# Kernel optimization log

Hardware: AMD Instinct MI355X
Metric: run time of the kernel (lower is better)

The kernel has to match this reference:

```python
import jax, jax.numpy as jnp
import numpy as np

KAPPA = -1.0          # negative curvature (Poincare ball, c = 1)
EPS = 1e-10
N, D_IN, D_OUT = 8192, 512, 512


def _artan_k(x):
    sc = np.sqrt(-KAPPA)
    return jnp.arctanh(jnp.clip(sc * x, -1.0 + 1e-7, 1.0 - 1e-7)) / sc


def _tan_k(x):
    sc = np.sqrt(-KAPPA)
    return jnp.tanh(sc * x) / sc


def _clamp_abs(x, eps=EPS):
    return jnp.where(x >= 0, 1.0, -1.0) * jnp.maximum(jnp.abs(x), eps)


def _norm(x):
    # stable last-dim L2 norm, clamped away from zero
    return jnp.sqrt(jnp.maximum(jnp.sum(x * x, axis=-1, keepdims=True), EPS * EPS))


def mobius_matvec(W, x):
    # geoopt-style Mobius matrix-vector product: scale x@W so that the
    # gyro-norm matches tan_k((|mx|/|x|) * artan_k(|x|))
    x_norm = _norm(x)                       # [N,1]
    mx = x @ W                              # [N,D_out]
    mx_norm = _norm(mx)
    res = _tan_k(mx_norm / x_norm * _artan_k(x_norm)) * (mx / mx_norm)
    return jnp.where(mx_norm <= EPS, 0.0, res)


def mobius_scalar_mul(r, x):
    x_norm = _norm(x)
    return _tan_k(r * _artan_k(x_norm)) * (x / x_norm)


def weighted_midpoint_lincomb(A, X):
    # weighted Frechet-mean-like midpoint with lincomb=True (geoopt semantics):
    # gamma_i = lambda_x = 2 / (1 + kappa * |x_i|^2)
    gamma = jnp.maximum(2.0 / (1.0 + KAPPA * jnp.sum(X * X, axis=-1, keepdims=True)), 1e-15)  # [N,1]
    denom = _clamp_abs(A @ (gamma - 1.0))   # [N,1]  (sum_j A_ij (gamma_j - 1))
    nom = A @ (gamma * X)                   # [N,D]  (sum_j A_ij gamma_j x_j)  -- GEMM, no NxNxD temp
    two_mean = nom / denom
    sq = jnp.sum(two_mean * two_mean, axis=-1, keepdims=True)
    a_mean = two_mean / (1.0 + jnp.sqrt(jnp.maximum(1.0 + KAPPA * sq, EPS)))
    alpha = jnp.sum(A, axis=-1, keepdims=True)   # lincomb: Mobius-scale by total weight
    return mobius_scalar_mul(alpha, a_mean)


def logmap0(x):
    xn = _norm(x)
    return _artan_k(xn) * x / xn


def expmap0(u):
    un = _norm(u)
    return _tan_k(un) * u / un


def setup_inputs() -> dict:
    key = jax.random.key(0)
    k1, k2, k3 = jax.random.split(key, 3)
    # node embeddings well inside the Poincare ball (|x| ~ 0.02)
    X = jax.random.normal(k1, (N, D_IN), dtype=jnp.float32) * 0.001
    # dense nonnegative normalized adjacency (rows sum ~ 0.5)
    A_hat = jax.random.uniform(k2, (N, N), dtype=jnp.float32) / N
    W = jax.random.normal(k3, (D_IN, D_OUT), dtype=jnp.float32) * 0.01
    return {"X": X, "A_hat": A_hat, "W": W}


def reference(X, A_hat, W):
    XW = mobius_matvec(W, X)                     # Mobius linear layer
    AXW = weighted_midpoint_lincomb(A_hat, XW)   # adjacency-weighted midpoint aggregation
    return expmap0(jax.nn.relu(logmap0(AXW)))    # sigma = exp0(relu(log0(.)))
```

## Files before the change

### kernel.cpp

```cpp
#include <hip/hip_runtime.h>


#define NR 8192
#define DD 512

typedef unsigned int u32;
typedef unsigned short u16;
typedef __attribute__((ext_vector_type(8))) short bf16x8;
typedef __attribute__((ext_vector_type(4))) float f32x4;

__device__ __forceinline__ u16 f2bf(float f) {
  u32 u = __float_as_uint(f);
  u32 r = u + 0x7FFFu + ((u >> 16) & 1u);
  return (u16)(r >> 16);
}

__device__ __forceinline__ u32 cvtpk(float lo, float hi) {
  u32 r;
  asm("v_cvt_pk_bf16_f32 %0, %1, %2" : "=v"(r) : "v"(lo), "v"(hi));
  return r;
}

__device__ __forceinline__ void gload16(const void* g, void* l) {
  __builtin_amdgcn_global_load_lds(
      (const __attribute__((address_space(1))) u32*)g,
      (__attribute__((address_space(3))) u32*)l, 16, 0, 0);
}

__device__ __forceinline__ float wred(float v) {
  #pragma unroll
  for (int off = 32; off; off >>= 1) v += __shfl_xor(v, off, 64);
  return v;
}

__global__ __launch_bounds__(256) void conv_wt(const float* __restrict__ W,
                                               u16* __restrict__ Wt) {
  const int idx = blockIdx.x * 256 + threadIdx.x;
  const int n  = idx >> 6;
  const int k0 = (idx & 63) * 8;
  u32 r[4];
  #pragma unroll
  for (int j = 0; j < 4; ++j) {
    float lo = W[(size_t)(k0 + 2*j    ) * DD + n];
    float hi = W[(size_t)(k0 + 2*j + 1) * DD + n];
    r[j] = (u32)f2bf(lo) | ((u32)f2bf(hi) << 16);
  }
  const int dst = n * DD + ((idx & 63) >> 2) * 32 + (((idx & 3) ^ (n & 3)) * 8);
  *(uint4*)(Wt + dst) = *(const uint4*)r;
}

template <int DOSUM>
__global__ __launch_bounds__(512, 2) void gemm_big(
    const float* __restrict__ Af, const u16* __restrict__ Bt,
    const u16* __restrict__ g1bf,
    float* __restrict__ C0, float* __restrict__ Cext,
    float* __restrict__ denp, float* __restrict__ alp,
    int M, int K, int kchunk, int nkc) {
  __shared__ __align__(16) float ldsA[2][4096];
  __shared__ __align__(16) u16   ldsB[2][16384];
  __shared__ __align__(16) u16   ldsG[2048];

  const int bid = blockIdx.x;
  int mt, kc;
  if (nkc == 1) { mt = bid; kc = 0; }
  else { kc = (bid & 7) >> 1; mt = ((bid >> 3) << 1) | (bid & 1); }

  const int t = threadIdx.x;
  const int lane = t & 63, w = t >> 6;
  const int wm = w >> 2, wn = w & 3;
  const int m0 = mt * 128;
  const int kbeg = kc * kchunk;
  const int lr = lane & 15, lk = lane >> 4, lx = lr & 7;

  const int Rb   = t >> 3;
  const int scol = ((t & 7) ^ (Rb & 7)) << 2;
  const float* gA0 = Af + (size_t)(m0 + Rb) * K + kbeg + scol;

  const u16* gB = Bt + (size_t)(t >> 2) * K + kbeg + (t & 3) * 8;

  auto stage = [&](int buf, int kt) {
    const int ko = kt * 32;
    #pragma unroll
    for (int j = 0; j < 2; ++j)
      gload16(gA0 + ko + (size_t)j * 64 * K, &ldsA[buf][t * 4 + j * 2048]);
    #pragma unroll
    for (int j = 0; j < 4; ++j)
      gload16(gB + ko + (size_t)j * 128 * K, &ldsB[buf][t * 8 + j * 4096]);
  };

  f32x4 acc[4][8];
  #pragma unroll
  for (int i = 0; i < 4; ++i)
    #pragma unroll
    for (int j = 0; j < 8; ++j) acc[i][j] = (f32x4){0.f, 0.f, 0.f, 0.f};
  f32x4 accS[4];
  #pragma unroll
  for (int i = 0; i < 4; ++i) accS[i] = (f32x4){0.f, 0.f, 0.f, 0.f};

  const int nT = kchunk / 32;

  if (DOSUM && w < 4) gload16(g1bf + kbeg + t * 8, &ldsG[t * 8]);
  stage(0, 0);
  stage(1, 1);
  asm volatile("s_waitcnt vmcnt(6)" ::: "memory");
  __builtin_amdgcn_s_barrier();
  __builtin_amdgcn_sched_barrier(0);

  int cur = 0;
  for (int tt = 0; tt < nT; ++tt) {
    bf16x8 af[4], bv[8];
    #pragma unroll
    for (int i = 0; i < 4; ++i) {
      const int rbase = (wm * 64 + i * 16 + lr) * 32;
      f32x4 lo = *(const f32x4*)&ldsA[cur][rbase + (((2*lk    ) ^ lx) << 2)];
      f32x4 hi = *(const f32x4*)&ldsA[cur][rbase + (((2*lk + 1) ^ lx) << 2)];
      union { u32 u[4]; bf16x8 v; } pk;
      pk.u[0] = cvtpk(lo.x, lo.y); pk.u[1] = cvtpk(lo.z, lo.w);
      pk.u[2] = cvtpk(hi.x, hi.y); pk.u[3] = cvtpk(hi.z, hi.w);
      af[i] = pk.v;
    }
    #pragma unroll
    for (int i = 0; i < 8; ++i) {
      const int rb = (wn * 128 + i * 16 + lr) * 32 + ((lk ^ (lr & 3)) << 3);
      bv[i] = *(const bf16x8*)&ldsB[cur][rb];
    }
    bf16x8 gv;
    if (DOSUM && wn == 0) {
      if (lr == 0) {
        gv = *(const bf16x8*)&ldsG[tt * 32 + lk * 8];
      } else {
        const short s = (lr == 1) ? (short)0x3F80 : (short)0;
        gv = (bf16x8){s, s, s, s, s, s, s, s};
      }
    }
    asm volatile("s_waitcnt lgkmcnt(0)" ::: "memory");
    __builtin_amdgcn_s_barrier();
    __builtin_amdgcn_sched_barrier(0);
    if (tt + 2 < nT) stage(cur, tt + 2);
    __builtin_amdgcn_sched_barrier(0);
    #pragma unroll
    for (int mi = 0; mi < 4; ++mi)
      #pragma unroll
      for (int ni = 0; ni < 8; ++ni)
        acc[mi][ni] = __builtin_amdgcn_mfma_f32_16x16x32_bf16(
            af[mi], bv[ni], acc[mi][ni], 0, 0, 0);
    if (DOSUM && wn == 0) {
      #pragma unroll
      for (int i = 0; i < 4; ++i)
        accS[i] = __builtin_amdgcn_mfma_f32_16x16x32_bf16(
            af[i], gv, accS[i], 0, 0, 0);
    }
    if (tt + 1 < nT) {
      __builtin_amdgcn_sched_barrier(0);
      if (tt + 2 < nT) {
        asm volatile("s_waitcnt vmcnt(6)" ::: "memory");
      } else {
        asm volatile("s_waitcnt vmcnt(0)" ::: "memory");
      }
      __builtin_amdgcn_s_barrier();
      __builtin_amdgcn_sched_barrier(0);
    }
    cur ^= 1;
  }

  if (DOSUM && wn == 0 && lr < 2) {
    float* dst = ((lr == 0) ? denp : alp) + (size_t)kc * M + m0 + wm * 64;
    #pragma unroll
    for (int i = 0; i < 4; ++i)
      #pragma unroll
      for (int v = 0; v < 4; ++v)
        dst[i * 16 + lk * 4 + v] = accS[i][v];
  }

  float* C = (kc == 0) ? C0 : (Cext + (size_t)(kc - 1) * M * DD);
  float* Cw = C + (size_t)(m0 + wm * 64 + lk * 4) * DD + wn * 128 + lr;
  #pragma unroll
  for (int mi = 0; mi < 4; ++mi)
    #pragma unroll
    for (int ni = 0; ni < 8; ++ni)
      #pragma unroll
      for (int v = 0; v < 4; ++v)
        Cw[(size_t)(mi * 16 + v) * DD + ni * 16] = acc[mi][ni][v];
}

__global__ __launch_bounds__(256) void rowstats(const float* __restrict__ X,
                                                const float* __restrict__ mx,
                                                float* __restrict__ fg,
                                                u16* __restrict__ g1bf) {
  const int row  = (blockIdx.x << 2) + (threadIdx.x >> 6);
  const int lane = threadIdx.x & 63;
  const float* xr = X  + (size_t)row * DD + lane * 8;
  const float* mr = mx + (size_t)row * DD + lane * 8;
  float4 a0 = *(const float4*)xr, a1 = *(const float4*)(xr + 4);
  float4 b0 = *(const float4*)mr, b1 = *(const float4*)(mr + 4);
  float sx = a0.x*a0.x + a0.y*a0.y + a0.z*a0.z + a0.w*a0.w
           + a1.x*a1.x + a1.y*a1.y + a1.z*a1.z + a1.w*a1.w;
  float sm = b0.x*b0.x + b0.y*b0.y + b0.z*b0.z + b0.w*b0.w
           + b1.x*b1.x + b1.y*b1.y + b1.z*b1.z + b1.w*b1.w;
  sx = wred(sx); sm = wred(sm);
  if (lane == 0) {
    float xn  = sqrtf(fmaxf(sx, 1e-20f));
    float mxn = sqrtf(fmaxf(sm, 1e-20f));
    float at  = atanhf(fminf(xn, 0.9999999f));
    float t_  = tanhf(mxn / xn * at);
    bool  z   = (mxn <= 1e-10f);
    float factor = z ? 0.f : t_ / mxn;
    float xwsq   = z ? 0.f : t_ * t_ * (sm / (mxn * mxn));
    float g = 2.f / (1.f - xwsq);
    g = fmaxf(g, 1e-15f);
    fg[row] = factor * g;
    g1bf[row] = f2bf(g - 1.f);
  }
}

__global__ __launch_bounds__(256) void build_bt(const float* __restrict__ mx,
                                                const float* __restrict__ fg,
                                                u16* __restrict__ Bt) {
  __shared__ float tile[64][65];
  const int j0 = blockIdx.x * 64, d0 = blockIdx.y * 64;
  const int t = threadIdx.x;
  const int r0 = t >> 4, c4 = (t & 15) * 4;
  #pragma unroll
  for (int p = 0; p < 4; ++p) {
    const int r = r0 + p * 16;
    const float s = fg[j0 + r];
    float4 v = *(const float4*)&mx[(size_t)(j0 + r) * DD + d0 + c4];
    tile[r][c4 + 0] = s * v.x; tile[r][c4 + 1] = s * v.y;
    tile[r][c4 + 2] = s * v.z; tile[r][c4 + 3] = s * v.w;
  }
  __syncthreads();
  const int dr = t >> 2, jc = (t & 3) * 16;
  u32 r[8];
  #pragma unroll
  for (int u = 0; u < 8; ++u) {
    float lo = tile[jc + 2 * u][dr];
    float hi = tile[jc + 2 * u + 1][dr];
    r[u] = (u32)f2bf(lo) | ((u32)f2bf(hi) << 16);
  }
  const int s0 = (jc >> 3) & 3;
  const int px = dr & 3;
  u32* rowp = (u32*)(Bt + (size_t)(d0 + dr) * NR + j0 + (jc & 32));
  *(uint4*)(rowp + ((s0 ^ px) * 4))       = *(const uint4*)&r[0];
  *(uint4*)(rowp + (((s0 + 1) ^ px) * 4)) = *(const uint4*)&r[4];
}

__global__ __launch_bounds__(256) void epilogue(const float* __restrict__ P0,
                                                const float* __restrict__ P1,
                                                const float* __restrict__ P2,
                                                const float* __restrict__ P3,
                                                const float* __restrict__ denp,
                                                const float* __restrict__ alp,
                                                float* __restrict__ out) {
  const int row  = (blockIdx.x << 2) + (threadIdx.x >> 6);
  const int lane = threadIdx.x & 63;
  const size_t ro = (size_t)row * DD + lane * 8;
  float4 n0 = *(const float4*)(P0 + ro), n1 = *(const float4*)(P0 + ro + 4);
  float4 a, b;
  a = *(const float4*)(P1 + ro); b = *(const float4*)(P1 + ro + 4);
  n0.x += a.x; n0.y += a.y; n0.z += a.z; n0.w += a.w;
  n1.x += b.x; n1.y += b.y; n1.z += b.z; n1.w += b.w;
  a = *(const float4*)(P2 + ro); b = *(const float4*)(P2 + ro + 4);
  n0.x += a.x; n0.y += a.y; n0.z += a.z; n0.w += a.w;
  n1.x += b.x; n1.y += b.y; n1.z += b.z; n1.w += b.w;
  a = *(const float4*)(P3 + ro); b = *(const float4*)(P3 + ro + 4);
  n0.x += a.x; n0.y += a.y; n0.z += a.z; n0.w += a.w;
  n1.x += b.x; n1.y += b.y; n1.z += b.z; n1.w += b.w;

  float de = 0.f, alpha = 0.f;
  #pragma unroll
  for (int kc = 0; kc < 4; ++kc) {
    de    += denp[kc * NR + row];
    alpha += alp [kc * NR + row];
  }
  de = (de >= 0.f ? 1.f : -1.f) * fmaxf(fabsf(de), 1e-10f);

  float v[8] = {n0.x / de, n0.y / de, n0.z / de, n0.w / de,
                n1.x / de, n1.y / de, n1.z / de, n1.w / de};
  float sq = 0.f;
  #pragma unroll
  for (int j = 0; j < 8; ++j) sq += v[j] * v[j];
  sq = wred(sq);
  float s1 = 1.f + sqrtf(fmaxf(1.f - sq, 1e-10f));
  float an = sqrtf(fmaxf(sq / (s1 * s1), 1e-20f));
  float t2 = tanhf(alpha * atanhf(fminf(an, 0.9999999f)));
  float f2 = t2 / (an * s1);
  float xsq = f2 * f2 * sq;
  float xn = sqrtf(fmaxf(xsq, 1e-20f));
  float lf = atanhf(fminf(xn, 0.9999999f)) / xn;
  float u[8]; float us = 0.f;
  #pragma unroll
  for (int j = 0; j < 8; ++j) {
    u[j] = fmaxf(lf * f2 * v[j], 0.f);
    us += u[j] * u[j];
  }
  us = wred(us);
  float un = sqrtf(fmaxf(us, 1e-20f));
  float ef = tanhf(un) / un;
  float o[8];
  #pragma unroll
  for (int j = 0; j < 8; ++j) o[j] = ef * u[j];
  float* orow = out + (size_t)row * DD + lane * 8;
  *(float4*)orow       = (float4){o[0], o[1], o[2], o[3]};
  *(float4*)(orow + 4) = (float4){o[4], o[5], o[6], o[7]};
}

extern "C" void kernel_launch(void* const* d_in, const int* in_sizes, int n_in,
                              void* d_out, int out_size, void* d_ws, size_t ws_size,
                              hipStream_t stream) {
  const float* X = (const float*)d_in[0];
  const float* A = (const float*)d_in[1];
  const float* W = (const float*)d_in[2];
  float* out = (float*)d_out;
  char* ws = (char*)d_ws;

  float* mx   = (float*)(ws);
  float* Pext = (float*)(ws + 16777216);
  u16*   Bt   = (u16*)(ws + 67108864);
  u16*   Wt   = (u16*)(ws + 75497472);
  float* fg   = (float*)(ws + 76021760);
  u16*   g1bf = (u16*)(ws + 76054528);
  float* denp = (float*)(ws + 76087296);
  float* alp  = (float*)(ws + 76218368);

  const size_t MNf = (size_t)NR * DD;

  conv_wt<<<128, 256, 0, stream>>>(W, Wt);
  gemm_big<0><<<64, 512, 0, stream>>>(X, Wt, g1bf, mx, mx, denp, alp,
                                      NR, DD, DD, 1);
  rowstats<<<2048, 256, 0, stream>>>(X, mx, fg, g1bf);
  build_bt<<<dim3(128, 8), 256, 0, stream>>>(mx, fg, Bt);
  gemm_big<1><<<256, 512, 0, stream>>>(A, Bt, g1bf, mx, Pext, denp, alp,
                                       NR, NR, NR / 4, 4);
  epilogue<<<2048, 256, 0, stream>>>(mx, Pext, Pext + MNf, Pext + 2 * MNf,
                                     denp, alp, out);
}
```

Measured before the change: 201.1 us.

## Split GEMM tiles across N halves, halve split-K, interleave MFMA with staging

The big GEMM now runs 256-thread blocks on 128x256 output tiles, splitting N into two halves and K into two chunks instead of four. This halves the partial-sum buffers the epilogue must read and sum. The main loop is split into two MFMA halves with raised wave priority, and the next tile's loads are issued between them so memory traffic overlaps compute. In exchange, each A tile is now loaded by two blocks (once per N half), which adds A-matrix traffic and changes occupancy.

```diff
diff --git a/kernel.cpp b/kernel.cpp
--- a/kernel.cpp
+++ b/kernel.cpp
@@ -50,42 +50,42 @@
 }
 
 template <int DOSUM>
-__global__ __launch_bounds__(512, 2) void gemm_big(
+__global__ __launch_bounds__(256, 2) void gemm_ph(
     const float* __restrict__ Af, const u16* __restrict__ Bt,
     const u16* __restrict__ g1bf,
     float* __restrict__ C0, float* __restrict__ Cext,
     float* __restrict__ denp, float* __restrict__ alp,
     int M, int K, int kchunk, int nkc) {
   __shared__ __align__(16) float ldsA[2][4096];
-  __shared__ __align__(16) u16   ldsB[2][16384];
-  __shared__ __align__(16) u16   ldsG[2048];
+  __shared__ __align__(16) u16   ldsB[2][8192];
+  __shared__ __align__(16) u16   ldsG[4096];
 
   const int bid = blockIdx.x;
-  int mt, kc;
-  if (nkc == 1) { mt = bid; kc = 0; }
-  else { kc = (bid & 7) >> 1; mt = ((bid >> 3) << 1) | (bid & 1); }
+  const int nt = bid & 1;
+  const int h  = bid >> 1;
+  const int kc = (nkc == 2) ? (h & 1) : 0;
+  const int mt = (nkc == 2) ? (h >> 1) : h;
 
   const int t = threadIdx.x;
   const int lane = t & 63, w = t >> 6;
-  const int wm = w >> 2, wn = w & 3;
-  const int m0 = mt * 128;
+  const int wm = w >> 1, wn = w & 1;
+  const int m0 = mt * 128, n0 = nt * 256;
   const int kbeg = kc * kchunk;
   const int lr = lane & 15, lk = lane >> 4, lx = lr & 7;
-
-  const int Rb   = t >> 3;
-  const int scol = ((t & 7) ^ (Rb & 7)) << 2;
-  const float* gA0 = Af + (size_t)(m0 + Rb) * K + kbeg + scol;
-
-  const u16* gB = Bt + (size_t)(t >> 2) * K + kbeg + (t & 3) * 8;
+  const bool doRS = DOSUM && (nt == 0);
+
+  const int scol = ((t & 7) ^ ((t >> 3) & 7)) << 2;
+  const float* gA0 = Af + (size_t)(m0 + (t >> 3)) * K + kbeg + scol;
+  const u16* gB = Bt + (size_t)(n0 + (t >> 2)) * K + kbeg + (t & 3) * 8;
 
   auto stage = [&](int buf, int kt) {
     const int ko = kt * 32;
     #pragma unroll
-    for (int j = 0; j < 2; ++j)
-      gload16(gA0 + ko + (size_t)j * 64 * K, &ldsA[buf][t * 4 + j * 2048]);
-    #pragma unroll
     for (int j = 0; j < 4; ++j)
-      gload16(gB + ko + (size_t)j * 128 * K, &ldsB[buf][t * 8 + j * 4096]);
+      gload16(gA0 + ko + (size_t)j * 32 * K, &ldsA[buf][t * 4 + j * 1024]);
+    #pragma unroll
+    for (int j = 0; j < 4; ++j)
+      gload16(gB + ko + (size_t)j * 64 * K, &ldsB[buf][t * 8 + j * 2048]);
   };
 
   f32x4 acc[4][8];
@@ -99,10 +99,14 @@
 
   const int nT = kchunk / 32;
 
-  if (DOSUM && w < 4) gload16(g1bf + kbeg + t * 8, &ldsG[t * 8]);
+  if (doRS) {
+    #pragma unroll
+    for (int j = 0; j < 2; ++j)
+      gload16(g1bf + kbeg + t * 8 + j * 2048, &ldsG[t * 8 + j * 2048]);
+  }
   stage(0, 0);
   stage(1, 1);
-  asm volatile("s_waitcnt vmcnt(6)" ::: "memory");
+  asm volatile("s_waitcnt vmcnt(8)" ::: "memory");
   __builtin_amdgcn_s_barrier();
   __builtin_amdgcn_sched_barrier(0);
 
@@ -124,8 +128,21 @@
       const int rb = (wn * 128 + i * 16 + lr) * 32 + ((lk ^ (lr & 3)) << 3);
       bv[i] = *(const bf16x8*)&ldsB[cur][rb];
     }
+    __builtin_amdgcn_s_setprio(1);
+    #pragma unroll
+    for (int mi = 0; mi < 4; ++mi)
+      #pragma unroll
+      for (int ni = 0; ni < 4; ++ni)
+        acc[mi][ni] = __builtin_amdgcn_mfma_f32_16x16x32_bf16(
+            af[mi], bv[ni], acc[mi][ni], 0, 0, 0);
+    __builtin_amdgcn_s_setprio(0);
+    asm volatile("s_waitcnt lgkmcnt(0)" ::: "memory");
+    __builtin_amdgcn_sched_barrier(0);
+    __builtin_amdgcn_s_barrier();
+    __builtin_amdgcn_sched_barrier(0);
+    if (tt + 2 < nT) stage(cur, tt + 2);
     bf16x8 gv;
-    if (DOSUM && wn == 0) {
+    if (doRS && wn == 0) {
       if (lr == 0) {
         gv = *(const bf16x8*)&ldsG[tt * 32 + lk * 8];
       } else {
@@ -133,27 +150,25 @@
         gv = (bf16x8){s, s, s, s, s, s, s, s};
       }
     }
-    asm volatile("s_waitcnt lgkmcnt(0)" ::: "memory");
-    __builtin_amdgcn_s_barrier();
     __builtin_amdgcn_sched_barrier(0);
-    if (tt + 2 < nT) stage(cur, tt + 2);
-    __builtin_amdgcn_sched_barrier(0);
+    __builtin_amdgcn_s_setprio(1);
     #pragma unroll
     for (int mi = 0; mi < 4; ++mi)
       #pragma unroll
-      for (int ni = 0; ni < 8; ++ni)
+      for (int ni = 4; ni < 8; ++ni)
         acc[mi][ni] = __builtin_amdgcn_mfma_f32_16x16x32_bf16(
             af[mi], bv[ni], acc[mi][ni], 0, 0, 0);
-    if (DOSUM && wn == 0) {
+    if (doRS && wn == 0) {
       #pragma unroll
       for (int i = 0; i < 4; ++i)
         accS[i] = __builtin_amdgcn_mfma_f32_16x16x32_bf16(
             af[i], gv, accS[i], 0, 0, 0);
     }
+    __builtin_amdgcn_s_setprio(0);
+    __builtin_amdgcn_sched_barrier(0);
     if (tt + 1 < nT) {
-      __builtin_amdgcn_sched_barrier(0);
-      if (tt + 2 < nT) {
-        asm volatile("s_waitcnt vmcnt(6)" ::: "memory");
+      if (tt + 3 < nT) {
+        asm volatile("s_waitcnt vmcnt(8)" ::: "memory");
       } else {
         asm volatile("s_waitcnt vmcnt(0)" ::: "memory");
       }
@@ -163,7 +178,7 @@
     cur ^= 1;
   }
 
-  if (DOSUM && wn == 0 && lr < 2) {
+  if (doRS && wn == 0 && lr < 2) {
     float* dst = ((lr == 0) ? denp : alp) + (size_t)kc * M + m0 + wm * 64;
     #pragma unroll
     for (int i = 0; i < 4; ++i)
@@ -172,8 +187,8 @@
         dst[i * 16 + lk * 4 + v] = accS[i][v];
   }
 
-  float* C = (kc == 0) ? C0 : (Cext + (size_t)(kc - 1) * M * DD);
-  float* Cw = C + (size_t)(m0 + wm * 64 + lk * 4) * DD + wn * 128 + lr;
+  float* C = (kc == 0) ? C0 : Cext;
+  float* Cw = C + (size_t)(m0 + wm * 64 + lk * 4) * DD + n0 + wn * 128 + lr;
   #pragma unroll
   for (int mi = 0; mi < 4; ++mi)
     #pragma unroll
@@ -246,8 +261,6 @@
 
 __global__ __launch_bounds__(256) void epilogue(const float* __restrict__ P0,
                                                 const float* __restrict__ P1,
-                                                const float* __restrict__ P2,
-                                                const float* __restrict__ P3,
                                                 const float* __restrict__ denp,
                                                 const float* __restrict__ alp,
                                                 float* __restrict__ out) {
@@ -255,23 +268,12 @@
   const int lane = threadIdx.x & 63;
   const size_t ro = (size_t)row * DD + lane * 8;
   float4 n0 = *(const float4*)(P0 + ro), n1 = *(const float4*)(P0 + ro + 4);
-  float4 a, b;
-  a = *(const float4*)(P1 + ro); b = *(const float4*)(P1 + ro + 4);
+  float4 a = *(const float4*)(P1 + ro), b = *(const float4*)(P1 + ro + 4);
   n0.x += a.x; n0.y += a.y; n0.z += a.z; n0.w += a.w;
   n1.x += b.x; n1.y += b.y; n1.z += b.z; n1.w += b.w;
-  a = *(const float4*)(P2 + ro); b = *(const float4*)(P2 + ro + 4);
-  n0.x += a.x; n0.y += a.y; n0.z += a.z; n0.w += a.w;
-  n1.x += b.x; n1.y += b.y; n1.z += b.z; n1.w += b.w;
-  a = *(const float4*)(P3 + ro); b = *(const float4*)(P3 + ro + 4);
-  n0.x += a.x; n0.y += a.y; n0.z += a.z; n0.w += a.w;
-  n1.x += b.x; n1.y += b.y; n1.z += b.z; n1.w += b.w;
-
-  float de = 0.f, alpha = 0.f;
-  #pragma unroll
-  for (int kc = 0; kc < 4; ++kc) {
-    de    += denp[kc * NR + row];
-    alpha += alp [kc * NR + row];
-  }
+
+  float de    = denp[row] + denp[NR + row];
+  float alpha = alp[row]  + alp[NR + row];
   de = (de >= 0.f ? 1.f : -1.f) * fmaxf(fabsf(de), 1e-10f);
 
   float v[8] = {n0.x / de, n0.y / de, n0.z / de, n0.w / de,
@@ -314,23 +316,20 @@
   char* ws = (char*)d_ws;
 
   float* mx   = (float*)(ws);
-  float* Pext = (float*)(ws + 16777216);
-  u16*   Bt   = (u16*)(ws + 67108864);
-  u16*   Wt   = (u16*)(ws + 75497472);
-  float* fg   = (float*)(ws + 76021760);
-  u16*   g1bf = (u16*)(ws + 76054528);
-  float* denp = (float*)(ws + 76087296);
-  float* alp  = (float*)(ws + 76218368);
-
-  const size_t MNf = (size_t)NR * DD;
+  float* P1   = (float*)(ws + 16777216);
+  u16*   Bt   = (u16*)(ws + 33554432);
+  u16*   Wt   = (u16*)(ws + 41943040);
+  float* fg   = (float*)(ws + 42467328);
+  u16*   g1bf = (u16*)(ws + 42500096);
+  float* denp = (float*)(ws + 42516480);
+  float* alp  = (float*)(ws + 42582016);
 
   conv_wt<<<128, 256, 0, stream>>>(W, Wt);
-  gemm_big<0><<<64, 512, 0, stream>>>(X, Wt, g1bf, mx, mx, denp, alp,
+  gemm_ph<0><<<128, 256, 0, stream>>>(X, Wt, g1bf, mx, mx, denp, alp,
                                       NR, DD, DD, 1);
   rowstats<<<2048, 256, 0, stream>>>(X, mx, fg, g1bf);
   build_bt<<<dim3(128, 8), 256, 0, stream>>>(mx, fg, Bt);
-  gemm_big<1><<<256, 512, 0, stream>>>(A, Bt, g1bf, mx, Pext, denp, alp,
-                                       NR, NR, NR / 4, 4);
-  epilogue<<<2048, 256, 0, stream>>>(mx, Pext, Pext + MNf, Pext + 2 * MNf,
-                                     denp, alp, out);
-}
+  gemm_ph<1><<<256, 256, 0, stream>>>(A, Bt, g1bf, mx, P1, denp, alp,
+                                      NR, NR, NR / 2, 2);
+  epilogue<<<2048, 256, 0, stream>>>(mx, P1, denp, alp, out);
+}
```

Result: slower. 233.2 us (+15.9%).
